# Kernel tuning notes

Hardware: AMD Instinct MI355X
Metric: run time of the kernel (lower is better)

Reference implementation:

```python
import jax, jax.numpy as jnp
import numpy as np

DT = 0.01  # time-grid spacing


def _get_A(ts, omega_sq, gamma_0, gamma_amp, omega_d):
    # ts: [...]; returns [..., 2, 2] system matrix A(t)
    gamma = gamma_0 * (1.0 + gamma_amp * jnp.sin(omega_d * ts))
    z = jnp.zeros_like(ts)
    o = jnp.ones_like(ts)
    row0 = jnp.stack([z, o], axis=-1)
    row1 = jnp.stack([-omega_sq * o, -gamma], axis=-1)
    return jnp.stack([row0, row1], axis=-2)


def _expm2x2(M):
    # Closed-form matrix exponential for batched 2x2 matrices [..., 2, 2].
    a, b = M[..., 0, 0], M[..., 0, 1]
    c, d = M[..., 1, 0], M[..., 1, 1]
    m = 0.5 * (a + d)                 # trace/2
    det = a * d - b * c
    delta = m * m - det               # discriminant
    s = jnp.sqrt(jnp.abs(delta))
    pos = delta >= 0
    small = s < 1e-6
    s_safe = jnp.where(small, 1.0, s)
    cosl = jnp.where(pos, jnp.cosh(s), jnp.cos(s))
    sinch = jnp.where(small, 1.0,
                      jnp.where(pos, jnp.sinh(s_safe), jnp.sin(s_safe)) / s_safe)
    I = jnp.eye(2, dtype=M.dtype)
    em = jnp.exp(m)[..., None, None]
    return em * (cosl[..., None, None] * I
                 + sinch[..., None, None] * (M - m[..., None, None] * I))


def setup_inputs() -> dict:
    key = jax.random.key(0)
    k1, = jax.random.split(key, 1)
    T, B = 8192, 4096
    t = jnp.arange(T, dtype=jnp.float32) * DT
    x0 = jax.random.normal(k1, (2, B), dtype=jnp.float32)
    return {
        "t": t,
        "x0": x0,
        "omega_sq": jnp.float32(1.2),
        "gamma_0": jnp.float32(0.35),
        "gamma_amp": jnp.float32(0.15),
        "omega_d": jnp.float32(1.1),
        "use_commutator": 1,
    }


def reference(t, x0, omega_sq, gamma_0, gamma_amp, omega_d, use_commutator):
    t0 = t[:-1]                      # [T-1]
    dt = t[1:] - t[:-1]              # [T-1]
    A0 = _get_A(t0, omega_sq, gamma_0, gamma_amp, omega_d)
    A_mid = _get_A(t0 + dt / 2, omega_sq, gamma_0, gamma_amp, omega_d)
    A1 = _get_A(t0 + dt, omega_sq, gamma_0, gamma_amp, omega_d)
    Omega = A_mid * dt[:, None, None]               # Magnus-1 term
    if use_commutator:
        comm = A0 @ A1 - A1 @ A0                    # [T-1, 2, 2]
        Omega = Omega + (dt ** 2 / 12.0)[:, None, None] * comm
    E = _expm2x2(Omega)                             # [T-1, 2, 2] propagators

    def step(x, Ei):
        xn = Ei @ x                                 # [2, B]
        return xn, xn

    _, ys = jax.lax.scan(step, x0, E)
    return jnp.concatenate([x0[None], ys], axis=0)  # [T, 2, B]
```

## Files before the change

### kernel.cpp

```cpp
#include <hip/hip_runtime.h>


struct M2 { float a, b, c, d; };

__device__ __forceinline__ M2 mmul(const M2& X, const M2& Y) {
    M2 r;
    r.a = X.a * Y.a + X.b * Y.c;
    r.b = X.a * Y.b + X.b * Y.d;
    r.c = X.c * Y.a + X.d * Y.c;
    r.d = X.c * Y.b + X.d * Y.d;
    return r;
}

__global__ void e_kernel(const float* __restrict__ t,
                         const float* __restrict__ p_w2,
                         const float* __restrict__ p_g0,
                         const float* __restrict__ p_ga,
                         const float* __restrict__ p_wd,
                         const int* __restrict__ p_uc,
                         float4* __restrict__ E, int T) {
    int n = blockIdx.x * blockDim.x + threadIdx.x;
    if (n >= T - 1) return;
    float w2 = *p_w2, g0 = *p_g0, ga = *p_ga, wd = *p_wd;
    int uc = *p_uc;

    float t0 = t[n], t1 = t[n + 1];
    float dt = t1 - t0;
    float tm = t0 + dt * 0.5f;

    float gam0 = g0 * (1.0f + ga * sinf(wd * t0));
    float gamm = g0 * (1.0f + ga * sinf(wd * tm));
    float gam1 = g0 * (1.0f + ga * sinf(wd * t1));

    float Oa = 0.0f;
    float Ob = dt;
    float Oc = -w2 * dt;
    float Od = -gamm * dt;
    if (uc) {
        float k = dt * dt * (1.0f / 12.0f);
        float del = gam0 - gam1;
        Ob += k * del;
        Oc += k * (w2 * del);
    }

    float m   = 0.5f * (Oa + Od);
    float det = Oa * Od - Ob * Oc;
    float delta = m * m - det;
    float s = sqrtf(fabsf(delta));
    bool pos = delta >= 0.0f;
    bool small_ = s < 1e-6f;
    float s_safe = small_ ? 1.0f : s;
    float cosl = pos ? coshf(s) : cosf(s);
    float sn   = pos ? sinhf(s_safe) : sinf(s_safe);
    float sinch = small_ ? 1.0f : sn / s_safe;
    float em = expf(m);

    float4 Ev;
    Ev.x = em * (cosl + sinch * (Oa - m));
    Ev.y = em * (sinch * Ob);
    Ev.z = em * (sinch * Oc);
    Ev.w = em * (cosl + sinch * (Od - m));
    E[n] = Ev;
}

__global__ __launch_bounds__(1024) void scan_kernel(const float4* __restrict__ E,
                                                    float4* __restrict__ P, int T) {
    __shared__ float4 lds[1024];
    const int j = threadIdx.x;
    const int base = j * 8;

    M2 S[8];
    #pragma unroll
    for (int mi = 0; mi < 8; ++mi) {
        int k = base + mi;
        M2 Mk;
        if (k < T - 1) {
            float4 e = E[k];
            Mk.a = e.x; Mk.b = e.y; Mk.c = e.z; Mk.d = e.w;
        } else {
            Mk.a = 1.0f; Mk.b = 0.0f; Mk.c = 0.0f; Mk.d = 1.0f;
        }
        S[mi] = (mi == 0) ? Mk : mmul(Mk, S[mi - 1]);
    }

    M2 acc = S[7];
    lds[j] = make_float4(acc.a, acc.b, acc.c, acc.d);
    for (int d = 1; d < 1024; d <<= 1) {
        __syncthreads();
        M2 prev;
        bool act = (j >= d);
        if (act) {
            float4 p = lds[j - d];
            prev.a = p.x; prev.b = p.y; prev.c = p.z; prev.d = p.w;
        }
        __syncthreads();
        if (act) {
            acc = mmul(acc, prev);
            lds[j] = make_float4(acc.a, acc.b, acc.c, acc.d);
        }
    }
    __syncthreads();

    M2 Bm;
    if (j == 0) { Bm.a = 1.0f; Bm.b = 0.0f; Bm.c = 0.0f; Bm.d = 1.0f; }
    else {
        float4 p = lds[j - 1];
        Bm.a = p.x; Bm.b = p.y; Bm.c = p.z; Bm.d = p.w;
    }

    if (j == 0) P[0] = make_float4(1.0f, 0.0f, 0.0f, 1.0f);
    #pragma unroll
    for (int mi = 0; mi < 8; ++mi) {
        int g = base + mi + 1;
        if (g < T) {
            M2 r = mmul(S[mi], Bm);
            P[g] = make_float4(r.a, r.b, r.c, r.d);
        }
    }
}

__global__ __launch_bounds__(256) void out_kernel(const float4* __restrict__ P,
                                                  const float* __restrict__ x0,
                                                  float* __restrict__ out, int B) {
    const int n = blockIdx.x;
    const float4 p = P[n];
    const float4* xr0 = (const float4*)x0;
    const float4* xr1 = xr0 + (B >> 2);
    float4* o = (float4*)(out + (size_t)n * (size_t)(2 * B));
    const int q = B >> 2;

    for (int g = threadIdx.x; g < q; g += blockDim.x) {
        float4 u = xr0[g];
        float4 v = xr1[g];
        float4 r0, r1;
        r0.x = p.x * u.x + p.y * v.x;
        r0.y = p.x * u.y + p.y * v.y;
        r0.z = p.x * u.z + p.y * v.z;
        r0.w = p.x * u.w + p.y * v.w;
        r1.x = p.z * u.x + p.w * v.x;
        r1.y = p.z * u.y + p.w * v.y;
        r1.z = p.z * u.z + p.w * v.z;
        r1.w = p.z * u.w + p.w * v.w;
        o[g]     = r0;
        o[q + g] = r1;
    }
}

extern "C" void kernel_launch(void* const* d_in, const int* in_sizes, int n_in,
                              void* d_out, int out_size, void* d_ws, size_t ws_size,
                              hipStream_t stream) {
    const float* t   = (const float*)d_in[0];
    const float* x0  = (const float*)d_in[1];
    const float* w2  = (const float*)d_in[2];
    const float* g0  = (const float*)d_in[3];
    const float* ga  = (const float*)d_in[4];
    const float* wd  = (const float*)d_in[5];
    const int*   uc  = (const int*)d_in[6];

    const int T = in_sizes[0];
    const int B = in_sizes[1] / 2;

    float4* E = (float4*)d_ws;
    float4* P = E + T;

    float* out = (float*)d_out;

    int nE = T - 1;
    e_kernel<<<(nE + 255) / 256, 256, 0, stream>>>(t, w2, g0, ga, wd, uc, E, T);
    scan_kernel<<<1, 1024, 0, stream>>>(E, P, T);
    out_kernel<<<T, 256, 0, stream>>>(P, x0, out, B);
}
```

Measured before the change: 283.3 us.

## Fuse propagator build into scan and batch output rows with nontemporal stores

Computes each 2x2 propagator inside the single-block scan kernel instead of in a separate kernel, which removes one launch and the round trip of E through global memory. The output kernel now handles four time rows per block and writes with nontemporal stores, so the x0 loads are reused across rows and cache pollution from the large output is reduced. The transcendental work now runs inside one block, which may lengthen the serial scan stage.

```diff
diff --git a/kernel.cpp b/kernel.cpp
--- a/kernel.cpp
+++ b/kernel.cpp
@@ -2,6 +2,8 @@
 
 
 struct M2 { float a, b, c, d; };
+
+typedef float f32x4 __attribute__((ext_vector_type(4)));
 
 __device__ __forceinline__ M2 mmul(const M2& X, const M2& Y) {
     M2 r;
@@ -12,18 +14,9 @@
     return r;
 }
 
-__global__ void e_kernel(const float* __restrict__ t,
-                         const float* __restrict__ p_w2,
-                         const float* __restrict__ p_g0,
-                         const float* __restrict__ p_ga,
-                         const float* __restrict__ p_wd,
-                         const int* __restrict__ p_uc,
-                         float4* __restrict__ E, int T) {
-    int n = blockIdx.x * blockDim.x + threadIdx.x;
-    if (n >= T - 1) return;
-    float w2 = *p_w2, g0 = *p_g0, ga = *p_ga, wd = *p_wd;
-    int uc = *p_uc;
-
+__device__ __forceinline__ M2 build_E(const float* __restrict__ t, int n,
+                                      float w2, float g0, float ga, float wd,
+                                      int uc) {
     float t0 = t[n], t1 = t[n + 1];
     float dt = t1 - t0;
     float tm = t0 + dt * 0.5f;
@@ -55,19 +48,27 @@
     float sinch = small_ ? 1.0f : sn / s_safe;
     float em = expf(m);
 
-    float4 Ev;
-    Ev.x = em * (cosl + sinch * (Oa - m));
-    Ev.y = em * (sinch * Ob);
-    Ev.z = em * (sinch * Oc);
-    Ev.w = em * (cosl + sinch * (Od - m));
-    E[n] = Ev;
+    M2 E;
+    E.a = em * (cosl + sinch * (Oa - m));
+    E.b = em * (sinch * Ob);
+    E.c = em * (sinch * Oc);
+    E.d = em * (cosl + sinch * (Od - m));
+    return E;
 }
 
-__global__ __launch_bounds__(1024) void scan_kernel(const float4* __restrict__ E,
-                                                    float4* __restrict__ P, int T) {
+__global__ __launch_bounds__(1024) void escan_kernel(const float* __restrict__ t,
+                                                     const float* __restrict__ p_w2,
+                                                     const float* __restrict__ p_g0,
+                                                     const float* __restrict__ p_ga,
+                                                     const float* __restrict__ p_wd,
+                                                     const int* __restrict__ p_uc,
+                                                     float4* __restrict__ P, int T) {
     __shared__ float4 lds[1024];
     const int j = threadIdx.x;
     const int base = j * 8;
+
+    float w2 = *p_w2, g0 = *p_g0, ga = *p_ga, wd = *p_wd;
+    int uc = *p_uc;
 
     M2 S[8];
     #pragma unroll
@@ -75,8 +76,7 @@
         int k = base + mi;
         M2 Mk;
         if (k < T - 1) {
-            float4 e = E[k];
-            Mk.a = e.x; Mk.b = e.y; Mk.c = e.z; Mk.d = e.w;
+            Mk = build_E(t, k, w2, g0, ga, wd, uc);
         } else {
             Mk.a = 1.0f; Mk.b = 0.0f; Mk.c = 0.0f; Mk.d = 1.0f;
         }
@@ -121,28 +121,34 @@
 
 __global__ __launch_bounds__(256) void out_kernel(const float4* __restrict__ P,
                                                   const float* __restrict__ x0,
-                                                  float* __restrict__ out, int B) {
-    const int n = blockIdx.x;
-    const float4 p = P[n];
+                                                  float* __restrict__ out,
+                                                  int B, int T) {
+    const int q = B >> 2;
     const float4* xr0 = (const float4*)x0;
-    const float4* xr1 = xr0 + (B >> 2);
-    float4* o = (float4*)(out + (size_t)n * (size_t)(2 * B));
-    const int q = B >> 2;
+    const float4* xr1 = xr0 + q;
+    const int n0 = blockIdx.x * 4;
 
-    for (int g = threadIdx.x; g < q; g += blockDim.x) {
-        float4 u = xr0[g];
-        float4 v = xr1[g];
-        float4 r0, r1;
-        r0.x = p.x * u.x + p.y * v.x;
-        r0.y = p.x * u.y + p.y * v.y;
-        r0.z = p.x * u.z + p.y * v.z;
-        r0.w = p.x * u.w + p.y * v.w;
-        r1.x = p.z * u.x + p.w * v.x;
-        r1.y = p.z * u.y + p.w * v.y;
-        r1.z = p.z * u.z + p.w * v.z;
-        r1.w = p.z * u.w + p.w * v.w;
-        o[g]     = r0;
-        o[q + g] = r1;
+    #pragma unroll
+    for (int nn = 0; nn < 4; ++nn) {
+        const int n = n0 + nn;
+        if (n >= T) return;
+        const float4 p = P[n];
+        float4* o = (float4*)(out + (size_t)n * (size_t)(2 * B));
+        for (int g = threadIdx.x; g < q; g += 256) {
+            float4 u = xr0[g];
+            float4 v = xr1[g];
+            float4 r0, r1;
+            r0.x = p.x * u.x + p.y * v.x;
+            r0.y = p.x * u.y + p.y * v.y;
+            r0.z = p.x * u.z + p.y * v.z;
+            r0.w = p.x * u.w + p.y * v.w;
+            r1.x = p.z * u.x + p.w * v.x;
+            r1.y = p.z * u.y + p.w * v.y;
+            r1.z = p.z * u.z + p.w * v.z;
+            r1.w = p.z * u.w + p.w * v.w;
+            __builtin_nontemporal_store(*(const f32x4*)&r0, (f32x4*)&o[g]);
+            __builtin_nontemporal_store(*(const f32x4*)&r1, (f32x4*)&o[q + g]);
+        }
     }
 }
 
@@ -160,13 +166,9 @@
     const int T = in_sizes[0];
     const int B = in_sizes[1] / 2;
 
-    float4* E = (float4*)d_ws;
-    float4* P = E + T;
-
+    float4* P = (float4*)d_ws;
     float* out = (float*)d_out;
 
-    int nE = T - 1;
-    e_kernel<<<(nE + 255) / 256, 256, 0, stream>>>(t, w2, g0, ga, wd, uc, E, T);
-    scan_kernel<<<1, 1024, 0, stream>>>(E, P, T);
-    out_kernel<<<T, 256, 0, stream>>>(P, x0, out, B);
+    escan_kernel<<<1, 1024, 0, stream>>>(t, w2, g0, ga, wd, uc, P, T);
+    out_kernel<<<(T + 3) / 4, 256, 0, stream>>>(P, x0, out, B, T);
 }
```

Measured after the change: 300.0 us. 5.9% more time.
